# Performance work log

Measured on AMD Instinct MI355X. Metric: run time of the kernel, lower is better.

## Reference

```python
import jax, jax.numpy as jnp
import numpy as np

N_NODES = 100000
N_EDGES = 1600000
D = 128
L = 3


def setup_inputs() -> dict:
    key = jax.random.key(0)
    k1, k2, k3 = jax.random.split(key, 3)
    edge_index = jax.random.randint(k1, (2, N_EDGES), 0, N_NODES, dtype=jnp.int64)
    emb = jax.random.normal(k2, (N_NODES, D), dtype=jnp.float32)
    # Glorot-style scale for the per-layer linear weights
    Ws = jax.random.normal(k3, (L, D, D), dtype=jnp.float32) * (1.0 / np.sqrt(D))
    bs = jnp.zeros((L, D), dtype=jnp.float32)
    return {"edge_index": edge_index, "emb": emb, "Ws": Ws, "bs": bs}


def _gcn_forward(emb, Ws, bs, edge_index):
    n = emb.shape[0]
    self_loop = jnp.arange(n, dtype=edge_index.dtype)
    # PyG GCNConv adds self-loops and uses symmetric normalization
    row = jnp.concatenate([edge_index[0], self_loop])  # source nodes
    col = jnp.concatenate([edge_index[1], self_loop])  # target nodes
    deg = jax.ops.segment_sum(jnp.ones(row.shape[0], dtype=emb.dtype), col, num_segments=n)
    deg_inv_sqrt = jnp.where(deg > 0, jax.lax.rsqrt(jnp.maximum(deg, 1.0)), 0.0)
    norm = deg_inv_sqrt[row] * deg_inv_sqrt[col]  # [E+N]

    x = emb
    for l in range(Ws.shape[0]):
        h = x @ Ws[l]                              # [N, D] linear transform
        msg = h[row] * norm[:, None]               # gather + scale [E+N, D]
        x = jax.ops.segment_sum(msg, col, num_segments=n) + bs[l]  # scatter-add
        x = jax.nn.relu(x)                         # dropout is identity in eval
    return x


def reference(edge_index, emb, Ws, bs) -> jnp.ndarray:
    return _gcn_forward(emb, Ws, bs, edge_index)
```

## Files before the change

### kernel.cpp

```cpp
#include <hip/hip_runtime.h>
#include <hip/hip_fp16.h>
#include <cstdint>
#include <cstddef>

#define N_NODES 100000
#define N_PAD 100096
#define N_EDGES 1600000
#define D 128
#define NLAYERS 3
#define NB 3125
#define NBLK_E 128
#define EPB 12500
#define ENT_CAP 1024

typedef float f2v __attribute__((ext_vector_type(2)));
typedef float f4v __attribute__((ext_vector_type(4)));
typedef _Float16 f16x8 __attribute__((ext_vector_type(8)));
typedef float f32x4 __attribute__((ext_vector_type(4)));
typedef unsigned u32x4 __attribute__((ext_vector_type(4)));


__global__ __launch_bounds__(512) void hist1_kernel(const int* __restrict__ col,
                                                    int* __restrict__ hmat) {
    __shared__ int hist[NB];
    int b = blockIdx.x, t = threadIdx.x;
    for (int j = t; j < NB; j += 512) hist[j] = 0;
    __syncthreads();
    int base = b * EPB;
    for (int i = t; i < EPB; i += 512) {
        int c = col[base + i];
        atomicAdd(&hist[c >> 5], 1);
    }
    __syncthreads();
    for (int j = t; j < NB; j += 512) hmat[b * NB + j] = hist[j];
}

__global__ void btot_kernel(const int* __restrict__ hmat, int* __restrict__ btot) {
    int j = blockIdx.x * 256 + threadIdx.x;
    if (j < NB) {
        int s = 0;
        for (int b = 0; b < NBLK_E; b++) s += hmat[b * NB + j];
        btot[j] = s;
    }
}

__global__ void bscan_kernel(const int* __restrict__ btot, int* __restrict__ bstart, int nb, int e) {
    __shared__ int lsum[1024];
    int t = threadIdx.x;
    int vals[4];
    int v0 = 0;
#pragma unroll
    for (int j = 0; j < 4; j++) {
        int idx = t * 4 + j;
        int c = (idx < nb) ? btot[idx] : 0;
        vals[j] = c;
        v0 += c;
    }
    lsum[t] = v0;
    __syncthreads();
    for (int off = 1; off < 1024; off <<= 1) {
        int x = (t >= off) ? lsum[t - off] : 0;
        __syncthreads();
        lsum[t] += x;
        __syncthreads();
    }
    int base = lsum[t] - v0;
#pragma unroll
    for (int j = 0; j < 4; j++) {
        int idx = t * 4 + j;
        if (idx < nb) {
            bstart[idx] = base;
            base += vals[j];
        }
    }
    if (t == 0) bstart[nb] = e;
}

__global__ void hoff_kernel(const int* __restrict__ hmat, const int* __restrict__ bstart,
                            int* __restrict__ hoff) {
    int j = blockIdx.x * 256 + threadIdx.x;
    if (j < NB) {
        int run = bstart[j];
        for (int b = 0; b < NBLK_E; b++) {
            hoff[b * NB + j] = run;
            run += hmat[b * NB + j];
        }
    }
}

__global__ __launch_bounds__(512) void scatter_kernel(const int* __restrict__ row,
                                                      const int* __restrict__ col,
                                                      const int* __restrict__ hoff,
                                                      unsigned* __restrict__ bucketbuf) {
    __shared__ int cur[NB];
    int b = blockIdx.x, t = threadIdx.x;
    for (int j = t; j < NB; j += 512) cur[j] = hoff[b * NB + j];
    __syncthreads();
    int base = b * EPB;
    for (int i = t; i < EPB; i += 512) {
        int r = row[base + i], c = col[base + i];
        int pos = atomicAdd(&cur[c >> 5], 1);
        bucketbuf[pos] = ((unsigned)r << 5) | (unsigned)(c & 31);
    }
}

__global__ void fill2_kernel(const unsigned* __restrict__ bucketbuf, const int* __restrict__ bstart,
                             int* __restrict__ offsets, float* __restrict__ dinv,
                             int* __restrict__ src, int n, int e) {
    __shared__ unsigned ent[ENT_CAP];
    __shared__ int hist[32];
    __shared__ int cur[32];
    __shared__ int loff[32];
    int b = blockIdx.x, t = threadIdx.x;
    int s0 = bstart[b];
    int cnt = bstart[b + 1] - s0;
    if (cnt > ENT_CAP) cnt = ENT_CAP;
    if (t < 32) hist[t] = 0;
    __syncthreads();
    for (int i = t; i < cnt; i += 256) {
        unsigned v = bucketbuf[s0 + i];
        ent[i] = v;
        atomicAdd(&hist[v & 31], 1);
    }
    __syncthreads();
    if (t == 0) {
        int run = s0;
#pragma unroll
        for (int j = 0; j < 32; j++) {
            loff[j] = run;
            run += hist[j];
        }
    }
    __syncthreads();
    if (t < 32) {
        int node = b * 32 + t;
        int o = loff[t];
        offsets[node] = o;
        cur[t] = o;
        dinv[node] = rsqrtf((float)(hist[t] + 1));
    }
    if (b == 0 && t == 0) offsets[n] = e;
    __syncthreads();
    for (int i = t; i < cnt; i += 256) {
        unsigned v = ent[i];
        int pos = atomicAdd(&cur[v & 31], 1);
        src[pos] = (int)(v >> 5);
    }
}


__global__ void cast_kernel(const float2* __restrict__ in, const float* __restrict__ dinv,
                            __half2* __restrict__ out, int n2) {
    int i = blockIdx.x * 256 + threadIdx.x;
    if (i < n2) {
        float d = dinv[i >> 6];
        float2 v = in[i];
        out[i] = __floats2half2_rn(d * v.x, d * v.y);
    }
}

__global__ void wsplit_kernel(const float* __restrict__ W,
                              _Float16* __restrict__ Wh, _Float16* __restrict__ Wl) {
    int c = blockIdx.x, l = blockIdx.y, k = threadIdx.x;
    float w = W[(size_t)l * 16384 + k * 128 + c];
    _Float16 h = (_Float16)w;
    float r = w - (float)h;
    Wh[(size_t)l * 16384 + c * 128 + k] = h;
    Wl[(size_t)l * 16384 + c * 128 + k] = (_Float16)r;
}

__global__ void agg_kernel(const __half2* __restrict__ xs, const int* __restrict__ offs,
                           unsigned* __restrict__ Ah, unsigned* __restrict__ Al,
                           const float* __restrict__ dinv, const int* __restrict__ src) {
    int v = blockIdx.x;
    int f = threadIdx.x;
    float dv = dinv[v];
    float2 a0 = __half22float2(xs[(size_t)v * 64 + f]);
    float ax = a0.x;
    float ay = a0.y;
    int i = offs[v], s1 = offs[v + 1];
    for (; i + 7 < s1; i += 8) {
        int s[8];
#pragma unroll
        for (int j = 0; j < 8; j++) s[j] = src[i + j];
        float2 x[8];
#pragma unroll
        for (int j = 0; j < 8; j++) x[j] = __half22float2(xs[(size_t)s[j] * 64 + f]);
#pragma unroll
        for (int j = 0; j < 8; j++) {
            ax += x[j].x;
            ay += x[j].y;
        }
    }
    if (i < s1) {
        int last = s1 - 1;
        int s[8];
        float m[8];
#pragma unroll
        for (int j = 0; j < 8; j++) {
            int idx = i + j;
            bool in = idx < s1;
            s[j] = src[in ? idx : last];
            m[j] = in ? 1.0f : 0.0f;
        }
        float2 x[8];
#pragma unroll
        for (int j = 0; j < 8; j++) x[j] = __half22float2(xs[(size_t)s[j] * 64 + f]);
#pragma unroll
        for (int j = 0; j < 8; j++) {
            ax += m[j] * x[j].x;
            ay += m[j] * x[j].y;
        }
    }
    float rx = dv * ax, ry = dv * ay;
    __half2 h2 = __floats2half2_rn(rx, ry);
    float2 hb = __half22float2(h2);
    __half2 l2 = __floats2half2_rn(rx - hb.x, ry - hb.y);
    __builtin_nontemporal_store(__builtin_bit_cast(unsigned, h2), Ah + (size_t)v * 64 + f);
    __builtin_nontemporal_store(__builtin_bit_cast(unsigned, l2), Al + (size_t)v * 64 + f);
}

__global__ __launch_bounds__(256) void gemm_mfma_kernel(
    const _Float16* __restrict__ Ahp, const _Float16* __restrict__ Alp,
    const _Float16* __restrict__ Whp, const _Float16* __restrict__ Wlp,
    const float* __restrict__ bias, float* __restrict__ out,
    __half2* __restrict__ xs_out, const float* __restrict__ dinv,
    int write_h, int write_out, int nrows) {
    __shared__ _Float16 sA[2][128][40];
    __shared__ _Float16 sW[2][128][40];
    int t = threadIdx.x;
    int lane = t & 63, wv = t >> 6;
    int lrow = lane & 15, kg = lane >> 4;
    int row0 = blockIdx.x * 128;

    f32x4 acc[2][8];
#pragma unroll
    for (int m = 0; m < 2; m++)
#pragma unroll
        for (int nn = 0; nn < 8; nn++) acc[m][nn] = (f32x4){0.f, 0.f, 0.f, 0.f};

    const u32x4* Aq[2] = {(const u32x4*)Ahp, (const u32x4*)Alp};
    const u32x4* Wq[2] = {(const u32x4*)Whp, (const u32x4*)Wlp};

    u32x4 av[4], wvr[4];

#define LOADCH(kc)                                                                    \
    {                                                                                 \
        _Pragma("unroll") for (int i = 0; i < 4; i++) {                               \
            int sid = t + 256 * i;                                                    \
            int p = i >> 1;                                                           \
            int rr = (sid >> 2) & 127;                                                \
            int k2 = sid & 3;                                                         \
            av[i] = __builtin_nontemporal_load(                                       \
                &Aq[p][(size_t)(row0 + rr) * 16 + (kc) * 4 + k2]);                    \
            wvr[i] = Wq[p][(size_t)rr * 16 + (kc) * 4 + k2];                          \
        }                                                                             \
    }

#define STORECH()                                                                     \
    {                                                                                 \
        _Pragma("unroll") for (int i = 0; i < 4; i++) {                               \
            int sid = t + 256 * i;                                                    \
            int p = i >> 1;                                                           \
            int rr = (sid >> 2) & 127;                                                \
            int k2 = sid & 3;                                                         \
            *(u32x4*)&sA[p][rr][k2 * 8] = av[i];                                      \
            *(u32x4*)&sW[p][rr][k2 * 8] = wvr[i];                                     \
        }                                                                             \
    }

    LOADCH(0);
#pragma unroll
    for (int kc = 0; kc < 4; kc++) {
        __syncthreads();
        STORECH();
        if (kc < 3) LOADCH(kc + 1);
        __syncthreads();

        f16x8 a0h = *(const f16x8*)&sA[0][wv * 32 + lrow][kg * 8];
        f16x8 a1h = *(const f16x8*)&sA[0][wv * 32 + 16 + lrow][kg * 8];
        f16x8 a0l = *(const f16x8*)&sA[1][wv * 32 + lrow][kg * 8];
        f16x8 a1l = *(const f16x8*)&sA[1][wv * 32 + 16 + lrow][kg * 8];
#pragma unroll
        for (int nn = 0; nn < 8; nn++) {
            f16x8 bh = *(const f16x8*)&sW[0][nn * 16 + lrow][kg * 8];
            f16x8 bl = *(const f16x8*)&sW[1][nn * 16 + lrow][kg * 8];
            acc[0][nn] = __builtin_amdgcn_mfma_f32_16x16x32_f16(a0h, bh, acc[0][nn], 0, 0, 0);
            acc[0][nn] = __builtin_amdgcn_mfma_f32_16x16x32_f16(a0l, bh, acc[0][nn], 0, 0, 0);
            acc[0][nn] = __builtin_amdgcn_mfma_f32_16x16x32_f16(a0h, bl, acc[0][nn], 0, 0, 0);
            acc[1][nn] = __builtin_amdgcn_mfma_f32_16x16x32_f16(a1h, bh, acc[1][nn], 0, 0, 0);
            acc[1][nn] = __builtin_amdgcn_mfma_f32_16x16x32_f16(a1l, bh, acc[1][nn], 0, 0, 0);
            acc[1][nn] = __builtin_amdgcn_mfma_f32_16x16x32_f16(a1h, bl, acc[1][nn], 0, 0, 0);
        }
    }
#undef LOADCH
#undef STORECH

    float bcolv[8];
#pragma unroll
    for (int nn = 0; nn < 8; nn++) bcolv[nn] = bias[nn * 16 + lrow];
#pragma unroll
    for (int m = 0; m < 2; m++) {
        int rbase = row0 + wv * 32 + m * 16 + kg * 4;
#pragma unroll
        for (int j = 0; j < 4; j++) {
            int rowi = rbase + j;
            bool ok = rowi < nrows;
            float dvr = (ok && write_h) ? dinv[rowi] : 0.f;
#pragma unroll
            for (int nn = 0; nn < 8; nn++) {
                float o = fmaxf(acc[m][nn][j] + bcolv[nn], 0.f);
                float o2 = __shfl_xor(o, 1);
                int col = nn * 16 + lrow;
                if (ok) {
                    if (write_out)
                        __builtin_nontemporal_store(o, out + (size_t)rowi * 128 + col);
                    if (write_h && !(lane & 1))
                        xs_out[(size_t)rowi * 64 + (col >> 1)] =
                            __floats2half2_rn(dvr * o, dvr * o2);
                }
            }
        }
    }
}


extern "C" void kernel_launch(void* const* d_in, const int* in_sizes, int n_in,
                              void* d_out, int out_size, void* d_ws, size_t ws_size,
                              hipStream_t stream) {
    const int* edge = (const int*)d_in[0];
    const float* emb = (const float*)d_in[1];
    const float* Ws = (const float*)d_in[2];
    const float* bs = (const float*)d_in[3];
    float* out = (float*)d_out;

    const int n = N_NODES, e = N_EDGES;
    const int* row = edge;
    const int* col = edge + e;

    char* p = (char*)d_ws;
    _Float16* Ah = (_Float16*)p;
    int* hmat = (int*)p;
    int* hoff = hmat + (size_t)NBLK_E * NB;
    p += (size_t)N_PAD * D * 2;
    _Float16* Al = (_Float16*)p;
    p += (size_t)N_PAD * D * 2;
    __half2* xs = (__half2*)p;
    unsigned* bucketbuf = (unsigned*)p;
    p += (size_t)n * D * 2;
    int* csr_src  = (int*)p;    p += (size_t)e * 4;
    float* dinv   = (float*)p;  p += (size_t)n * 4;
    int* offsets  = (int*)p;    p += (size_t)(n + 1) * 4;
    int* btot     = (int*)p;    p += (size_t)NB * 4;
    int* bstart   = (int*)p;    p += (size_t)(NB + 1) * 4;
    _Float16* WhT = (_Float16*)p; p += (size_t)NLAYERS * D * D * 2;
    _Float16* WlT = (_Float16*)p; p += (size_t)NLAYERS * D * D * 2;

    hist1_kernel<<<NBLK_E, 512, 0, stream>>>(col, hmat);
    btot_kernel<<<(NB + 255) / 256, 256, 0, stream>>>(hmat, btot);
    bscan_kernel<<<1, 1024, 0, stream>>>(btot, bstart, NB, e);
    hoff_kernel<<<(NB + 255) / 256, 256, 0, stream>>>(hmat, bstart, hoff);
    scatter_kernel<<<NBLK_E, 512, 0, stream>>>(row, col, hoff, bucketbuf);
    fill2_kernel<<<NB, 256, 0, stream>>>(bucketbuf, bstart, offsets, dinv, csr_src, n, e);
    wsplit_kernel<<<dim3(128, NLAYERS), 128, 0, stream>>>(Ws, WhT, WlT);

    int n2 = n * 64;
    cast_kernel<<<(n2 + 255) / 256, 256, 0, stream>>>((const float2*)emb, dinv, xs, n2);

    const int ngb = N_PAD / 128;
    for (int l = 0; l < NLAYERS; l++) {
        agg_kernel<<<n, 64, 0, stream>>>(xs, offsets, (unsigned*)Ah, (unsigned*)Al,
                                         dinv, csr_src);
        gemm_mfma_kernel<<<ngb, 256, 0, stream>>>(
            Ah, Al, WhT + (size_t)l * D * D, WlT + (size_t)l * D * D,
            bs + (size_t)l * D, out, xs, dinv,
            (l < NLAYERS - 1) ? 1 : 0, (l == NLAYERS - 1) ? 1 : 0, n);
    }
}
```

Before: 493.7 us.

## Fuse neighbor aggregation and MFMA linear transform into one per-layer kernel

```diff
diff --git a/kernel.cpp b/kernel.cpp
--- a/kernel.cpp
+++ b/kernel.cpp
@@ -4,7 +4,6 @@
 #include <cstddef>
 
 #define N_NODES 100000
-#define N_PAD 100096
 #define N_EDGES 1600000
 #define D 128
 #define NLAYERS 3
@@ -17,7 +16,6 @@
 typedef float f4v __attribute__((ext_vector_type(4)));
 typedef _Float16 f16x8 __attribute__((ext_vector_type(8)));
 typedef float f32x4 __attribute__((ext_vector_type(4)));
-typedef unsigned u32x4 __attribute__((ext_vector_type(4)));
 
 
 __global__ __launch_bounds__(512) void hist1_kernel(const int* __restrict__ col,
@@ -169,157 +167,109 @@
     Wl[(size_t)l * 16384 + c * 128 + k] = (_Float16)r;
 }
 
-__global__ void agg_kernel(const __half2* __restrict__ xs, const int* __restrict__ offs,
-                           unsigned* __restrict__ Ah, unsigned* __restrict__ Al,
-                           const float* __restrict__ dinv, const int* __restrict__ src) {
-    int v = blockIdx.x;
-    int f = threadIdx.x;
-    float dv = dinv[v];
-    float2 a0 = __half22float2(xs[(size_t)v * 64 + f]);
-    float ax = a0.x;
-    float ay = a0.y;
-    int i = offs[v], s1 = offs[v + 1];
-    for (; i + 7 < s1; i += 8) {
-        int s[8];
-#pragma unroll
-        for (int j = 0; j < 8; j++) s[j] = src[i + j];
-        float2 x[8];
-#pragma unroll
-        for (int j = 0; j < 8; j++) x[j] = __half22float2(xs[(size_t)s[j] * 64 + f]);
-#pragma unroll
-        for (int j = 0; j < 8; j++) {
-            ax += x[j].x;
-            ay += x[j].y;
-        }
-    }
-    if (i < s1) {
-        int last = s1 - 1;
-        int s[8];
-        float m[8];
-#pragma unroll
-        for (int j = 0; j < 8; j++) {
-            int idx = i + j;
-            bool in = idx < s1;
-            s[j] = src[in ? idx : last];
-            m[j] = in ? 1.0f : 0.0f;
-        }
-        float2 x[8];
-#pragma unroll
-        for (int j = 0; j < 8; j++) x[j] = __half22float2(xs[(size_t)s[j] * 64 + f]);
-#pragma unroll
-        for (int j = 0; j < 8; j++) {
-            ax += m[j] * x[j].x;
-            ay += m[j] * x[j].y;
-        }
-    }
-    float rx = dv * ax, ry = dv * ay;
-    __half2 h2 = __floats2half2_rn(rx, ry);
-    float2 hb = __half22float2(h2);
-    __half2 l2 = __floats2half2_rn(rx - hb.x, ry - hb.y);
-    __builtin_nontemporal_store(__builtin_bit_cast(unsigned, h2), Ah + (size_t)v * 64 + f);
-    __builtin_nontemporal_store(__builtin_bit_cast(unsigned, l2), Al + (size_t)v * 64 + f);
-}
-
-__global__ __launch_bounds__(256) void gemm_mfma_kernel(
-    const _Float16* __restrict__ Ahp, const _Float16* __restrict__ Alp,
+__global__ __launch_bounds__(64, 4) void agg_gemm_kernel(
+    const __half2* __restrict__ xs_in, const int* __restrict__ offs,
+    const int* __restrict__ src, const float* __restrict__ dinv,
     const _Float16* __restrict__ Whp, const _Float16* __restrict__ Wlp,
     const float* __restrict__ bias, float* __restrict__ out,
-    __half2* __restrict__ xs_out, const float* __restrict__ dinv,
-    int write_h, int write_out, int nrows) {
-    __shared__ _Float16 sA[2][128][40];
-    __shared__ _Float16 sW[2][128][40];
-    int t = threadIdx.x;
-    int lane = t & 63, wv = t >> 6;
-    int lrow = lane & 15, kg = lane >> 4;
-    int row0 = blockIdx.x * 128;
-
-    f32x4 acc[2][8];
-#pragma unroll
-    for (int m = 0; m < 2; m++)
-#pragma unroll
-        for (int nn = 0; nn < 8; nn++) acc[m][nn] = (f32x4){0.f, 0.f, 0.f, 0.f};
-
-    const u32x4* Aq[2] = {(const u32x4*)Ahp, (const u32x4*)Alp};
-    const u32x4* Wq[2] = {(const u32x4*)Whp, (const u32x4*)Wlp};
-
-    u32x4 av[4], wvr[4];
-
-#define LOADCH(kc)                                                                    \
-    {                                                                                 \
-        _Pragma("unroll") for (int i = 0; i < 4; i++) {                               \
-            int sid = t + 256 * i;                                                    \
-            int p = i >> 1;                                                           \
-            int rr = (sid >> 2) & 127;                                                \
-            int k2 = sid & 3;                                                         \
-            av[i] = __builtin_nontemporal_load(                                       \
-                &Aq[p][(size_t)(row0 + rr) * 16 + (kc) * 4 + k2]);                    \
-            wvr[i] = Wq[p][(size_t)rr * 16 + (kc) * 4 + k2];                          \
-        }                                                                             \
-    }
-
-#define STORECH()                                                                     \
-    {                                                                                 \
-        _Pragma("unroll") for (int i = 0; i < 4; i++) {                               \
-            int sid = t + 256 * i;                                                    \
-            int p = i >> 1;                                                           \
-            int rr = (sid >> 2) & 127;                                                \
-            int k2 = sid & 3;                                                         \
-            *(u32x4*)&sA[p][rr][k2 * 8] = av[i];                                      \
-            *(u32x4*)&sW[p][rr][k2 * 8] = wvr[i];                                     \
-        }                                                                             \
-    }
-
-    LOADCH(0);
-#pragma unroll
-    for (int kc = 0; kc < 4; kc++) {
-        __syncthreads();
-        STORECH();
-        if (kc < 3) LOADCH(kc + 1);
-        __syncthreads();
-
-        f16x8 a0h = *(const f16x8*)&sA[0][wv * 32 + lrow][kg * 8];
-        f16x8 a1h = *(const f16x8*)&sA[0][wv * 32 + 16 + lrow][kg * 8];
-        f16x8 a0l = *(const f16x8*)&sA[1][wv * 32 + lrow][kg * 8];
-        f16x8 a1l = *(const f16x8*)&sA[1][wv * 32 + 16 + lrow][kg * 8];
-#pragma unroll
-        for (int nn = 0; nn < 8; nn++) {
-            f16x8 bh = *(const f16x8*)&sW[0][nn * 16 + lrow][kg * 8];
-            f16x8 bl = *(const f16x8*)&sW[1][nn * 16 + lrow][kg * 8];
-            acc[0][nn] = __builtin_amdgcn_mfma_f32_16x16x32_f16(a0h, bh, acc[0][nn], 0, 0, 0);
-            acc[0][nn] = __builtin_amdgcn_mfma_f32_16x16x32_f16(a0l, bh, acc[0][nn], 0, 0, 0);
-            acc[0][nn] = __builtin_amdgcn_mfma_f32_16x16x32_f16(a0h, bl, acc[0][nn], 0, 0, 0);
-            acc[1][nn] = __builtin_amdgcn_mfma_f32_16x16x32_f16(a1h, bh, acc[1][nn], 0, 0, 0);
-            acc[1][nn] = __builtin_amdgcn_mfma_f32_16x16x32_f16(a1l, bh, acc[1][nn], 0, 0, 0);
-            acc[1][nn] = __builtin_amdgcn_mfma_f32_16x16x32_f16(a1h, bl, acc[1][nn], 0, 0, 0);
-        }
-    }
-#undef LOADCH
-#undef STORECH
-
-    float bcolv[8];
-#pragma unroll
-    for (int nn = 0; nn < 8; nn++) bcolv[nn] = bias[nn * 16 + lrow];
-#pragma unroll
-    for (int m = 0; m < 2; m++) {
-        int rbase = row0 + wv * 32 + m * 16 + kg * 4;
-#pragma unroll
-        for (int j = 0; j < 4; j++) {
-            int rowi = rbase + j;
-            bool ok = rowi < nrows;
-            float dvr = (ok && write_h) ? dinv[rowi] : 0.f;
-#pragma unroll
-            for (int nn = 0; nn < 8; nn++) {
-                float o = fmaxf(acc[m][nn][j] + bcolv[nn], 0.f);
-                float o2 = __shfl_xor(o, 1);
-                int col = nn * 16 + lrow;
-                if (ok) {
-                    if (write_out)
-                        __builtin_nontemporal_store(o, out + (size_t)rowi * 128 + col);
-                    if (write_h && !(lane & 1))
-                        xs_out[(size_t)rowi * 64 + (col >> 1)] =
-                            __floats2half2_rn(dvr * o, dvr * o2);
-                }
+    __half2* __restrict__ xs_out, int write_h, int write_out) {
+    __shared__ _Float16 sA[2][16][136];
+    int f = threadIdx.x;
+    int r0 = blockIdx.x * 16;
+
+#pragma unroll 1
+    for (int lr = 0; lr < 16; lr++) {
+        int v = r0 + lr;
+        float dv = dinv[v];
+        float2 a0 = __half22float2(xs_in[(size_t)v * 64 + f]);
+        float ax = a0.x;
+        float ay = a0.y;
+        int i = offs[v], s1 = offs[v + 1];
+        for (; i + 7 < s1; i += 8) {
+            int s[8];
+#pragma unroll
+            for (int j = 0; j < 8; j++) s[j] = src[i + j];
+            float2 x[8];
+#pragma unroll
+            for (int j = 0; j < 8; j++) x[j] = __half22float2(xs_in[(size_t)s[j] * 64 + f]);
+#pragma unroll
+            for (int j = 0; j < 8; j++) {
+                ax += x[j].x;
+                ay += x[j].y;
             }
+        }
+        if (i < s1) {
+            int last = s1 - 1;
+            int s[8];
+            float m[8];
+#pragma unroll
+            for (int j = 0; j < 8; j++) {
+                int idx = i + j;
+                bool in = idx < s1;
+                s[j] = src[in ? idx : last];
+                m[j] = in ? 1.0f : 0.0f;
+            }
+            float2 x[8];
+#pragma unroll
+            for (int j = 0; j < 8; j++) x[j] = __half22float2(xs_in[(size_t)s[j] * 64 + f]);
+#pragma unroll
+            for (int j = 0; j < 8; j++) {
+                ax += m[j] * x[j].x;
+                ay += m[j] * x[j].y;
+            }
+        }
+        float rx = dv * ax, ry = dv * ay;
+        __half2 h2 = __floats2half2_rn(rx, ry);
+        float2 hb = __half22float2(h2);
+        __half2 l2 = __floats2half2_rn(rx - hb.x, ry - hb.y);
+        *(unsigned*)&sA[0][lr][2 * f] = __builtin_bit_cast(unsigned, h2);
+        *(unsigned*)&sA[1][lr][2 * f] = __builtin_bit_cast(unsigned, l2);
+    }
+    __syncthreads();
+
+    int lrow = f & 15, kg = f >> 4;
+    f32x4 acc[8];
+#pragma unroll
+    for (int nf = 0; nf < 8; nf++) acc[nf] = (f32x4){0.f, 0.f, 0.f, 0.f};
+
+#pragma unroll
+    for (int ks = 0; ks < 4; ks++) {
+        int g = ks * 4 + kg;
+        f16x8 ah = *(const f16x8*)&sA[0][lrow][g * 8];
+        f16x8 al = *(const f16x8*)&sA[1][lrow][g * 8];
+#pragma unroll
+        for (int nf = 0; nf < 8; nf++) {
+            int col = nf * 16 + lrow;
+            f16x8 bh = *(const f16x8*)&Whp[(size_t)col * 128 + g * 8];
+            acc[nf] = __builtin_amdgcn_mfma_f32_16x16x32_f16(ah, bh, acc[nf], 0, 0, 0);
+            acc[nf] = __builtin_amdgcn_mfma_f32_16x16x32_f16(al, bh, acc[nf], 0, 0, 0);
+        }
+#pragma unroll
+        for (int nf = 0; nf < 8; nf++) {
+            int col = nf * 16 + lrow;
+            f16x8 bl = *(const f16x8*)&Wlp[(size_t)col * 128 + g * 8];
+            acc[nf] = __builtin_amdgcn_mfma_f32_16x16x32_f16(ah, bl, acc[nf], 0, 0, 0);
+        }
+    }
+
+    float bcol[8];
+#pragma unroll
+    for (int nf = 0; nf < 8; nf++) bcol[nf] = bias[nf * 16 + lrow];
+    int rbase = r0 + kg * 4;
+#pragma unroll
+    for (int j = 0; j < 4; j++) {
+        int rowi = rbase + j;
+        float dvr = write_h ? dinv[rowi] : 0.f;
+#pragma unroll
+        for (int nf = 0; nf < 8; nf++) {
+            float o = fmaxf(acc[nf][j] + bcol[nf], 0.f);
+            float o2 = __shfl_xor(o, 1);
+            int col = nf * 16 + lrow;
+            if (write_out)
+                __builtin_nontemporal_store(o, out + (size_t)rowi * 128 + col);
+            if (write_h && !(f & 1))
+                xs_out[(size_t)rowi * 64 + (col >> 1)] =
+                    __floats2half2_rn(dvr * o, dvr * o2);
         }
     }
 }
@@ -339,20 +289,18 @@
     const int* col = edge + e;
 
     char* p = (char*)d_ws;
-    _Float16* Ah = (_Float16*)p;
-    int* hmat = (int*)p;
-    int* hoff = hmat + (size_t)NBLK_E * NB;
-    p += (size_t)N_PAD * D * 2;
-    _Float16* Al = (_Float16*)p;
-    p += (size_t)N_PAD * D * 2;
-    __half2* xs = (__half2*)p;
+    __half2* xsA = (__half2*)p;
     unsigned* bucketbuf = (unsigned*)p;
+    p += (size_t)n * D * 2;
+    __half2* xsB = (__half2*)p;
     p += (size_t)n * D * 2;
     int* csr_src  = (int*)p;    p += (size_t)e * 4;
     float* dinv   = (float*)p;  p += (size_t)n * 4;
     int* offsets  = (int*)p;    p += (size_t)(n + 1) * 4;
     int* btot     = (int*)p;    p += (size_t)NB * 4;
     int* bstart   = (int*)p;    p += (size_t)(NB + 1) * 4;
+    int* hmat     = (int*)p;    p += (size_t)NBLK_E * NB * 4;
+    int* hoff     = (int*)p;    p += (size_t)NBLK_E * NB * 4;
     _Float16* WhT = (_Float16*)p; p += (size_t)NLAYERS * D * D * 2;
     _Float16* WlT = (_Float16*)p; p += (size_t)NLAYERS * D * D * 2;
 
@@ -365,15 +313,16 @@
     wsplit_kernel<<<dim3(128, NLAYERS), 128, 0, stream>>>(Ws, WhT, WlT);
 
     int n2 = n * 64;
-    cast_kernel<<<(n2 + 255) / 256, 256, 0, stream>>>((const float2*)emb, dinv, xs, n2);
-
-    const int ngb = N_PAD / 128;
+    cast_kernel<<<(n2 + 255) / 256, 256, 0, stream>>>((const float2*)emb, dinv, xsA, n2);
+
+    __half2* xin = xsA;
+    __half2* xout = xsB;
     for (int l = 0; l < NLAYERS; l++) {
-        agg_kernel<<<n, 64, 0, stream>>>(xs, offsets, (unsigned*)Ah, (unsigned*)Al,
-                                         dinv, csr_src);
-        gemm_mfma_kernel<<<ngb, 256, 0, stream>>>(
-            Ah, Al, WhT + (size_t)l * D * D, WlT + (size_t)l * D * D,
-            bs + (size_t)l * D, out, xs, dinv,
-            (l < NLAYERS - 1) ? 1 : 0, (l == NLAYERS - 1) ? 1 : 0, n);
-    }
-}
+        agg_gemm_kernel<<<n / 16, 64, 0, stream>>>(
+            xin, offsets, csr_src, dinv,
+            WhT + (size_t)l * D * D, WlT + (size_t)l * D * D,
+            bs + (size_t)l * D, out, xout,
+            (l < NLAYERS - 1) ? 1 : 0, (l == NLAYERS - 1) ? 1 : 0);
+        __half2* tmp = xin; xin = xout; xout = tmp;
+    }
+}
```

Measured after the change: 544.7 us. 10.3% more time.
